# Optimization experiments

Measured on AMD Instinct MI355X. Metric: run time of the kernel, lower is better.

Reference implementation:

```python
import jax, jax.numpy as jnp
import numpy as np

N = 50000        # nodes
E = 1_600_000    # edges (avg degree 32)
D_IN = 128
HID = 256
D_OUT = 128      # must equal D_IN for the residual add


def setup_inputs() -> dict:
    key = jax.random.key(0)
    k0, k1, k2, k3 = jax.random.split(key, 4)
    x = jax.random.normal(k0, (N, D_IN), dtype=jnp.float32)
    edge_index = jax.random.randint(k1, (2, E), 0, N, dtype=jnp.int32)
    # GCNConv params (lin: Linear without bias in PyG, plus additive bias)
    W1 = jax.random.normal(k2, (D_IN, HID), dtype=jnp.float32) / np.sqrt(D_IN)
    b1 = jnp.zeros((HID,), jnp.float32)
    W2 = jax.random.normal(k3, (HID, D_OUT), dtype=jnp.float32) / np.sqrt(HID)
    b2 = jnp.zeros((D_OUT,), jnp.float32)
    return {"x": x, "edge_index": edge_index, "W1": W1, "b1": b1, "W2": W2, "b2": b2}


def _gcn_conv(x, src, dst, norm, W, b, n):
    # PyG GCNConv: transform, gather source features, scale by sym-norm, scatter-add to dst.
    h = x @ W                        # [n, d_out]
    msg = h[src] * norm[:, None]     # [E+n, d_out] gathered messages
    out = jax.ops.segment_sum(msg, dst, num_segments=n)
    return out + b


def reference(x, edge_index, W1, b1, W2, b2):
    n = x.shape[0]
    # add self loops (GCNConv default add_self_loops=True)
    loops = jnp.arange(n, dtype=edge_index.dtype)
    src = jnp.concatenate([edge_index[0], loops])
    dst = jnp.concatenate([edge_index[1], loops])
    # symmetric normalization D^{-1/2} (A+I) D^{-1/2}
    deg = jax.ops.segment_sum(jnp.ones_like(dst, dtype=x.dtype), dst, num_segments=n)
    dinv = jnp.where(deg > 0, jax.lax.rsqrt(deg), 0.0)
    norm = dinv[src] * dinv[dst]
    skip = x  # nn.Identity skip connection
    h = jax.nn.relu(_gcn_conv(x, src, dst, norm, W1, b1, n))
    out = _gcn_conv(h, src, dst, norm, W2, b2, n)
    # classification_layer treated as identity; original .double() cast kept in fp32
    return out + skip
```

## Files before the change

### kernel.cpp

```cpp
#include <hip/hip_runtime.h>

#define D_IN 128
#define HID 256
#define BKT_SHIFT 6
#define BKT_SIZE 64
#define BKT_CAP 3072
#define NBKT_MAX 1024
#define CHUNK 4096
#define PAD_SLACK 512
#define LSTR 264
#define ASTR 136

typedef __attribute__((ext_vector_type(8))) short short8;
typedef __attribute__((ext_vector_type(4))) float floatx4;
typedef __attribute__((ext_vector_type(4))) int intx4;

static __device__ __forceinline__ unsigned short f2b(float f) {
  unsigned u = __float_as_uint(f);
  unsigned r = (u + 0x7fffu + ((u >> 16) & 1u)) >> 16;
  return (unsigned short)r;
}

static __device__ __forceinline__ void unpack8(uint4 v, float* f) {
  f[0] = __uint_as_float(v.x << 16); f[1] = __uint_as_float(v.x & 0xffff0000u);
  f[2] = __uint_as_float(v.y << 16); f[3] = __uint_as_float(v.y & 0xffff0000u);
  f[4] = __uint_as_float(v.z << 16); f[5] = __uint_as_float(v.z & 0xffff0000u);
  f[6] = __uint_as_float(v.w << 16); f[7] = __uint_as_float(v.w & 0xffff0000u);
}

static __device__ __forceinline__ void acc_fma(float* acc, uint4 v, float w) {
  float g[8];
  unpack8(v, g);
#pragma unroll
  for (int d = 0; d < 8; ++d) acc[d] = fmaf(g[d], w, acc[d]);
}

static __device__ __forceinline__ void gather_row(float* acc, const uint4* __restrict__ Hq,
                                                  const float* __restrict__ dinv,
                                                  const int* __restrict__ csr,
                                                  int2 se, float dv, int lane) {
  intx4 c0 = *(const intx4*)(csr + se.x);
  intx4 c1 = *(const intx4*)(csr + se.x + 4);
  for (int j = se.x; j < se.y; ) {
    const int jn = j + 8;
    const int jp = (jn < se.y) ? jn : se.x;
    intx4 n0 = *(const intx4*)(csr + jp);
    intx4 n1 = *(const intx4*)(csr + jp + 4);
    float w0 = dinv[c0.x] * dv, w1 = dinv[c0.y] * dv;
    float w2 = dinv[c0.z] * dv, w3 = dinv[c0.w] * dv;
    float w4 = dinv[c1.x] * dv, w5 = dinv[c1.y] * dv;
    float w6 = dinv[c1.z] * dv, w7 = dinv[c1.w] * dv;
    uint4 v0 = Hq[(size_t)c0.x * 16 + lane];
    uint4 v1 = Hq[(size_t)c0.y * 16 + lane];
    uint4 v2 = Hq[(size_t)c0.z * 16 + lane];
    uint4 v3 = Hq[(size_t)c0.w * 16 + lane];
    uint4 v4 = Hq[(size_t)c1.x * 16 + lane];
    uint4 v5 = Hq[(size_t)c1.y * 16 + lane];
    uint4 v6 = Hq[(size_t)c1.z * 16 + lane];
    uint4 v7 = Hq[(size_t)c1.w * 16 + lane];
    acc_fma(acc, v0, w0);
    acc_fma(acc, v1, w1);
    acc_fma(acc, v2, w2);
    acc_fma(acc, v3, w3);
    acc_fma(acc, v4, w4);
    acc_fma(acc, v5, w5);
    acc_fma(acc, v6, w6);
    acc_fma(acc, v7, w7);
    c0 = n0; c1 = n1; j = jn;
  }
}


__global__ __launch_bounds__(256) void fused_front_kernel(
    const int* __restrict__ src, const int* __restrict__ dst,
    int* __restrict__ bkt_cursor, int* __restrict__ ebuf, int E, int nbkt, int nchunk,
    const float4* __restrict__ x4, unsigned short* __restrict__ xb, int n4,
    const float* __restrict__ W1, unsigned short* __restrict__ Wt1,
    const float* __restrict__ W2, unsigned short* __restrict__ Wt2,
    float* __restrict__ dinv, unsigned short* __restrict__ tb, int N) {
  const int bid = blockIdx.x;
  const int tid = threadIdx.x;
  if (bid < nchunk) {
    __shared__ int hist[NBKT_MAX];
    __shared__ int bbase[NBKT_MAX];
    for (int b = tid; b < nbkt; b += 256) hist[b] = 0;
    __syncthreads();
    const int base = bid * CHUNK;
    const int end = min(base + CHUNK, E);
    for (int e = base + tid; e < end; e += 256)
      atomicAdd(&hist[dst[e] >> BKT_SHIFT], 1);
    __syncthreads();
    for (int b = tid; b < nbkt; b += 256) {
      int c = hist[b];
      bbase[b] = c > 0 ? atomicAdd(&bkt_cursor[b], c) : 0;
      hist[b] = 0;
    }
    __syncthreads();
    for (int e = base + tid; e < end; e += 256) {
      int d = dst[e];
      int b = d >> BKT_SHIFT;
      int off = atomicAdd(&hist[b], 1);
      int rel = bbase[b] + off;
      if (rel < BKT_CAP)
        ebuf[b * BKT_CAP + rel] = (src[e] << BKT_SHIFT) | (d & (BKT_SIZE - 1));
    }
    return;
  }
  const int nxblk = (n4 + 255) / 256;
  if (bid < nchunk + nxblk) {
    int i = (bid - nchunk) * 256 + tid;
    if (i >= n4) return;
    float4 v = x4[i];
    ushort4 o;
    o.x = f2b(v.x); o.y = f2b(v.y); o.z = f2b(v.z); o.w = f2b(v.w);
    *(ushort4*)(xb + (size_t)i * 4) = o;
  } else if (bid < nchunk + nxblk + 128) {
    int e = (bid - nchunk - nxblk) * 256 + tid;
    int k = e >> 8, n = e & 255;
    Wt1[(size_t)n * D_IN + k] = f2b(W1[e]);
  } else if (bid < nchunk + nxblk + 256) {
    int e = (bid - nchunk - nxblk - 128) * 256 + tid;
    int k = e >> 7, n = e & 127;
    Wt2[(size_t)n * HID + k] = f2b(W2[e]);
  } else {
    if (tid == 0) dinv[N] = 0.f;
    if (tid < 64)       ((unsigned*)(xb + (size_t)N * D_IN))[tid]      = 0u;
    else if (tid < 128) ((unsigned*)(tb + (size_t)N * D_IN))[tid - 64] = 0u;
  }
}


__global__ __launch_bounds__(256) void bucket_build_kernel(const int* __restrict__ ebuf,
                                                           const int* __restrict__ bkt_cursor,
                                                           float* __restrict__ dinv,
                                                           int2* __restrict__ rowse,
                                                           int* __restrict__ csr,
                                                           int N, int nbkt) {
  __shared__ int hist[BKT_SIZE];
  __shared__ int srs[BKT_SIZE];
  const int b = blockIdx.x;
  const int tid = threadIdx.x;
  const int node0 = b << BKT_SHIFT;
  const int nloc = min(BKT_SIZE, N - node0);
  const int ebeg = b * BKT_CAP;
  const int eend = ebeg + min(bkt_cursor[b], BKT_CAP);

  if (tid < BKT_SIZE) hist[tid] = 0;
  __syncthreads();
  for (int e = ebeg + tid; e < eend; e += 256)
    atomicAdd(&hist[ebuf[e] & (BKT_SIZE - 1)], 1);
  __syncthreads();

  if (tid < BKT_SIZE) {
    const int h = hist[tid];
    const int p = (h + 7) & ~7;
    int incl = p;
#pragma unroll
    for (int off = 1; off < 64; off <<= 1) {
      int t = __shfl_up(incl, off);
      if (tid >= off) incl += t;
    }
    const int ex = incl - p;
    if (tid < nloc) {
      int st = b * (BKT_CAP + PAD_SLACK) + ex;
      dinv[node0 + tid] = rsqrtf((float)(h + 1));
      rowse[node0 + tid] = make_int2(st, st + p);
      srs[tid] = st;
    }
  }
  __syncthreads();
  if (tid < BKT_SIZE) hist[tid] = 0;
  __syncthreads();

  for (int e = ebeg + tid; e < eend; e += 256) {
    int u = ebuf[e];
    int l = u & (BKT_SIZE - 1);
    int pos = atomicAdd(&hist[l], 1);
    csr[srs[l] + pos] = u >> BKT_SHIFT;
  }
  __syncthreads();
  for (int l = tid; l < nloc; l += 256) {
    int deg = hist[l];
    int pp = (deg + 7) & ~7;
    int s0 = srs[l];
    for (int q = s0 + deg; q < s0 + pp; ++q) csr[q] = N;
  }
}


__global__ __launch_bounds__(512, 4) void agg1_gemm_kernel(
    const uint4* __restrict__ Hq, const int2* __restrict__ rowse,
    const int* __restrict__ csr, const float* __restrict__ dinv,
    const unsigned short* __restrict__ Wt1, const float* __restrict__ b1,
    const unsigned short* __restrict__ Wt2, unsigned short* __restrict__ T, int M) {
  __shared__ unsigned short as_[32][ASTR];
  __shared__ unsigned short hs[32][LSTR];
  const int tid = threadIdx.x;
  const int node0 = blockIdx.x * 32;

  {
    const int glane = tid & 15;
    const int lrow = tid >> 4;
    const int node = node0 + lrow;
    float acc[8] = {0.f, 0.f, 0.f, 0.f, 0.f, 0.f, 0.f, 0.f};
    if (node < M) {
      const float dv = dinv[node];
      uint4 sv = Hq[(size_t)node * 16 + glane];
      float f[8];
      unpack8(sv, f);
      const float ws = dv * dv;
#pragma unroll
      for (int d = 0; d < 8; ++d) acc[d] = f[d] * ws;
      gather_row(acc, Hq, dinv, csr, rowse[node], dv, glane);
    }
    uint4 o;
    o.x = (unsigned)f2b(acc[0]) | ((unsigned)f2b(acc[1]) << 16);
    o.y = (unsigned)f2b(acc[2]) | ((unsigned)f2b(acc[3]) << 16);
    o.z = (unsigned)f2b(acc[4]) | ((unsigned)f2b(acc[5]) << 16);
    o.w = (unsigned)f2b(acc[6]) | ((unsigned)f2b(acc[7]) << 16);
    *(uint4*)&as_[lrow][glane * 8] = o;
  }
  __syncthreads();

  const int wave = tid >> 6;
  const int lane = tid & 63;
  const int quad = lane >> 4;
  const int l16 = lane & 15;

  const short8* bp1 = (const short8*)(Wt1 + (size_t)(wave * 32 + l16) * D_IN + quad * 8);
  floatx4 acc1[2][2];
#pragma unroll
  for (int g = 0; g < 2; ++g)
#pragma unroll
    for (int t = 0; t < 2; ++t) acc1[g][t] = floatx4{0.f, 0.f, 0.f, 0.f};

#pragma unroll
  for (int kt = 0; kt < 4; ++kt) {
    short8 a0 = *(const short8*)&as_[0 * 16 + l16][kt * 32 + quad * 8];
    short8 a1 = *(const short8*)&as_[1 * 16 + l16][kt * 32 + quad * 8];
#pragma unroll
    for (int t = 0; t < 2; ++t) {
      short8 b = bp1[kt * 4 + t * 256];
      acc1[0][t] = __builtin_amdgcn_mfma_f32_16x16x32_bf16(a0, b, acc1[0][t], 0, 0, 0);
      acc1[1][t] = __builtin_amdgcn_mfma_f32_16x16x32_bf16(a1, b, acc1[1][t], 0, 0, 0);
    }
  }
#pragma unroll
  for (int t = 0; t < 2; ++t) {
    const float bv = b1[wave * 32 + t * 16 + l16];
#pragma unroll
    for (int g = 0; g < 2; ++g)
#pragma unroll
      for (int r = 0; r < 4; ++r) {
        float v = acc1[g][t][r] + bv;
        v = v > 0.f ? v : 0.f;
        hs[g * 16 + quad * 4 + r][wave * 32 + t * 16 + l16] = f2b(v);
      }
  }
  __syncthreads();

  const short8* bp2 = (const short8*)(Wt2 + (size_t)(wave * 16 + l16) * HID + quad * 8);
  floatx4 acc2[2];
#pragma unroll
  for (int g = 0; g < 2; ++g) acc2[g] = floatx4{0.f, 0.f, 0.f, 0.f};

#pragma unroll
  for (int kt = 0; kt < 8; ++kt) {
    short8 a0 = *(const short8*)&hs[0 * 16 + l16][kt * 32 + quad * 8];
    short8 a1 = *(const short8*)&hs[1 * 16 + l16][kt * 32 + quad * 8];
    short8 b = bp2[kt * 4];
    acc2[0] = __builtin_amdgcn_mfma_f32_16x16x32_bf16(a0, b, acc2[0], 0, 0, 0);
    acc2[1] = __builtin_amdgcn_mfma_f32_16x16x32_bf16(a1, b, acc2[1], 0, 0, 0);
  }
  __syncthreads();

#pragma unroll
  for (int g = 0; g < 2; ++g)
#pragma unroll
    for (int r = 0; r < 4; ++r)
      hs[g * 16 + quad * 4 + r][wave * 16 + l16] = f2b(acc2[g][r]);
  __syncthreads();

  {
    const int r = tid >> 4;
    const int c = (tid & 15) * 8;
    const int row = node0 + r;
    uint4 v = *(const uint4*)&hs[r][c];
    if (row < M) *(uint4*)&T[(size_t)row * D_IN + c] = v;
  }
}


__global__ __launch_bounds__(256) void agg2_kernel(const uint4* __restrict__ Hq,
                                                   const int2* __restrict__ rowse,
                                                   const int* __restrict__ csr,
                                                   const float* __restrict__ dinv,
                                                   const float* __restrict__ skip,
                                                   const float* __restrict__ bias,
                                                   float* __restrict__ OUT, int n) {
  const int lane = threadIdx.x & 15;
  const int node = blockIdx.x * 16 + (threadIdx.x >> 4);
  if (node >= n) return;

  const float dv = dinv[node];
  float acc[8];
  {
    uint4 sv = Hq[(size_t)node * 16 + lane];
    float f[8];
    unpack8(sv, f);
    const float ws = dv * dv;
#pragma unroll
    for (int d = 0; d < 8; ++d) acc[d] = f[d] * ws;
  }
  gather_row(acc, Hq, dinv, csr, rowse[node], dv, lane);

  const float* sp = skip + (size_t)node * 128 + lane * 8;
  const float* bp = bias + lane * 8;
  float4 s0 = *(const float4*)sp, s1 = *(const float4*)(sp + 4);
  float4 b0 = *(const float4*)bp, b1 = *(const float4*)(bp + 4);
  float* op = OUT + (size_t)node * 128 + lane * 8;
  *(float4*)op = make_float4(acc[0] + s0.x + b0.x, acc[1] + s0.y + b0.y,
                             acc[2] + s0.z + b0.z, acc[3] + s0.w + b0.w);
  *(float4*)(op + 4) = make_float4(acc[4] + s1.x + b1.x, acc[5] + s1.y + b1.y,
                                   acc[6] + s1.z + b1.z, acc[7] + s1.w + b1.w);
}


extern "C" void kernel_launch(void* const* d_in, const int* in_sizes, int n_in,
                              void* d_out, int out_size, void* d_ws, size_t ws_size,
                              hipStream_t stream) {
  const float* x  = (const float*)d_in[0];
  const int*   ei = (const int*)d_in[1];
  const float* W1 = (const float*)d_in[2];
  const float* b1 = (const float*)d_in[3];
  const float* W2 = (const float*)d_in[4];
  const float* b2 = (const float*)d_in[5];
  float* out = (float*)d_out;

  const int N = in_sizes[0] / D_IN;
  const int E = in_sizes[1] / 2;
  const int* srcA = ei;
  const int* dstA = ei + E;
  const int NBKT = (N + BKT_SIZE - 1) >> BKT_SHIFT;
  const int NCHUNK = (E + CHUNK - 1) / CHUNK;
  const int n4 = N * D_IN / 4;

  char* ws = (char*)d_ws;
  size_t off = 0;
  auto alloc = [&](size_t bytes) { void* p = ws + off; off = (off + bytes + 255) & ~(size_t)255; return p; };
  int*            bkt_cursor = (int*)           alloc((size_t)NBKT * 4);
  float*          dinv       = (float*)         alloc((size_t)(N + 1) * 4);
  int2*           rowse      = (int2*)          alloc((size_t)N * 8);
  int*            ebuf       = (int*)           alloc((size_t)NBKT * BKT_CAP * 4);
  int*            csr        = (int*)           alloc((size_t)NBKT * (BKT_CAP + PAD_SLACK) * 4);
  unsigned short* xb         = (unsigned short*)alloc((size_t)(N + 1) * D_IN * 2);
  unsigned short* tb         = (unsigned short*)alloc((size_t)(N + 1) * D_IN * 2);
  unsigned short* Wt1        = (unsigned short*)alloc((size_t)D_IN * HID * 2);
  unsigned short* Wt2        = (unsigned short*)alloc((size_t)D_IN * HID * 2);

  const int nxblk = (n4 + 255) / 256;

  (void)hipMemsetAsync(bkt_cursor, 0, (size_t)NBKT * 4, stream);
  fused_front_kernel<<<NCHUNK + nxblk + 256 + 1, 256, 0, stream>>>(
      srcA, dstA, bkt_cursor, ebuf, E, NBKT, NCHUNK,
      (const float4*)x, xb, n4, W1, Wt1, W2, Wt2, dinv, tb, N);
  bucket_build_kernel<<<NBKT, 256, 0, stream>>>(ebuf, bkt_cursor, dinv, rowse, csr, N, NBKT);
  agg1_gemm_kernel<<<(N + 31) / 32, 512, 0, stream>>>((const uint4*)xb, rowse, csr, dinv,
                                                      Wt1, b1, Wt2, tb, N);
  agg2_kernel<<<(N + 15) / 16, 256, 0, stream>>>((const uint4*)tb, rowse, csr,
                                                 dinv, x, b2, out, N);
}
```

Measured before the change: 267.2 us.

## Prescale features by dinv so edge gathers become plain sums

Factors the symmetric normalization as dinv[dst]*sum(dinv[src]*h[src]). Source rows are prescaled by dinv when they are written (x during bucket build, layer-2 input in the GEMM epilogue), and the destination factor is applied once per row. This removes the per-edge dinv gathers and multiplies from both aggregation kernels. The x-to-bf16 conversion moves from the front kernel into bucket_build, where dinv is already in shared memory. The cost is slightly different rounding, since scaling now happens before bf16 quantization.

```diff
diff --git a/kernel.cpp b/kernel.cpp
--- a/kernel.cpp
+++ b/kernel.cpp
@@ -28,17 +28,16 @@
   f[6] = __uint_as_float(v.w << 16); f[7] = __uint_as_float(v.w & 0xffff0000u);
 }
 
-static __device__ __forceinline__ void acc_fma(float* acc, uint4 v, float w) {
+static __device__ __forceinline__ void acc_add(float* acc, uint4 v) {
   float g[8];
   unpack8(v, g);
 #pragma unroll
-  for (int d = 0; d < 8; ++d) acc[d] = fmaf(g[d], w, acc[d]);
+  for (int d = 0; d < 8; ++d) acc[d] += g[d];
 }
 
 static __device__ __forceinline__ void gather_row(float* acc, const uint4* __restrict__ Hq,
-                                                  const float* __restrict__ dinv,
                                                   const int* __restrict__ csr,
-                                                  int2 se, float dv, int lane) {
+                                                  int2 se, int lane) {
   intx4 c0 = *(const intx4*)(csr + se.x);
   intx4 c1 = *(const intx4*)(csr + se.x + 4);
   for (int j = se.x; j < se.y; ) {
@@ -46,10 +45,6 @@
     const int jp = (jn < se.y) ? jn : se.x;
     intx4 n0 = *(const intx4*)(csr + jp);
     intx4 n1 = *(const intx4*)(csr + jp + 4);
-    float w0 = dinv[c0.x] * dv, w1 = dinv[c0.y] * dv;
-    float w2 = dinv[c0.z] * dv, w3 = dinv[c0.w] * dv;
-    float w4 = dinv[c1.x] * dv, w5 = dinv[c1.y] * dv;
-    float w6 = dinv[c1.z] * dv, w7 = dinv[c1.w] * dv;
     uint4 v0 = Hq[(size_t)c0.x * 16 + lane];
     uint4 v1 = Hq[(size_t)c0.y * 16 + lane];
     uint4 v2 = Hq[(size_t)c0.z * 16 + lane];
@@ -58,14 +53,14 @@
     uint4 v5 = Hq[(size_t)c1.y * 16 + lane];
     uint4 v6 = Hq[(size_t)c1.z * 16 + lane];
     uint4 v7 = Hq[(size_t)c1.w * 16 + lane];
-    acc_fma(acc, v0, w0);
-    acc_fma(acc, v1, w1);
-    acc_fma(acc, v2, w2);
-    acc_fma(acc, v3, w3);
-    acc_fma(acc, v4, w4);
-    acc_fma(acc, v5, w5);
-    acc_fma(acc, v6, w6);
-    acc_fma(acc, v7, w7);
+    acc_add(acc, v0);
+    acc_add(acc, v1);
+    acc_add(acc, v2);
+    acc_add(acc, v3);
+    acc_add(acc, v4);
+    acc_add(acc, v5);
+    acc_add(acc, v6);
+    acc_add(acc, v7);
     c0 = n0; c1 = n1; j = jn;
   }
 }
@@ -74,10 +69,10 @@
 __global__ __launch_bounds__(256) void fused_front_kernel(
     const int* __restrict__ src, const int* __restrict__ dst,
     int* __restrict__ bkt_cursor, int* __restrict__ ebuf, int E, int nbkt, int nchunk,
-    const float4* __restrict__ x4, unsigned short* __restrict__ xb, int n4,
     const float* __restrict__ W1, unsigned short* __restrict__ Wt1,
     const float* __restrict__ W2, unsigned short* __restrict__ Wt2,
-    float* __restrict__ dinv, unsigned short* __restrict__ tb, int N) {
+    float* __restrict__ dinv, unsigned short* __restrict__ xb,
+    unsigned short* __restrict__ tb, int N) {
   const int bid = blockIdx.x;
   const int tid = threadIdx.x;
   if (bid < nchunk) {
@@ -106,20 +101,12 @@
     }
     return;
   }
-  const int nxblk = (n4 + 255) / 256;
-  if (bid < nchunk + nxblk) {
-    int i = (bid - nchunk) * 256 + tid;
-    if (i >= n4) return;
-    float4 v = x4[i];
-    ushort4 o;
-    o.x = f2b(v.x); o.y = f2b(v.y); o.z = f2b(v.z); o.w = f2b(v.w);
-    *(ushort4*)(xb + (size_t)i * 4) = o;
-  } else if (bid < nchunk + nxblk + 128) {
-    int e = (bid - nchunk - nxblk) * 256 + tid;
+  if (bid < nchunk + 128) {
+    int e = (bid - nchunk) * 256 + tid;
     int k = e >> 8, n = e & 255;
     Wt1[(size_t)n * D_IN + k] = f2b(W1[e]);
-  } else if (bid < nchunk + nxblk + 256) {
-    int e = (bid - nchunk - nxblk - 128) * 256 + tid;
+  } else if (bid < nchunk + 256) {
+    int e = (bid - nchunk - 128) * 256 + tid;
     int k = e >> 7, n = e & 127;
     Wt2[(size_t)n * HID + k] = f2b(W2[e]);
   } else {
@@ -132,12 +119,15 @@
 
 __global__ __launch_bounds__(256) void bucket_build_kernel(const int* __restrict__ ebuf,
                                                            const int* __restrict__ bkt_cursor,
+                                                           const float4* __restrict__ x4,
+                                                           unsigned short* __restrict__ xb,
                                                            float* __restrict__ dinv,
                                                            int2* __restrict__ rowse,
                                                            int* __restrict__ csr,
                                                            int N, int nbkt) {
   __shared__ int hist[BKT_SIZE];
   __shared__ int srs[BKT_SIZE];
+  __shared__ float sdinv[BKT_SIZE];
   const int b = blockIdx.x;
   const int tid = threadIdx.x;
   const int node0 = b << BKT_SHIFT;
@@ -161,9 +151,11 @@
       if (tid >= off) incl += t;
     }
     const int ex = incl - p;
+    float dv = rsqrtf((float)(h + 1));
+    sdinv[tid] = dv;
     if (tid < nloc) {
       int st = b * (BKT_CAP + PAD_SLACK) + ex;
-      dinv[node0 + tid] = rsqrtf((float)(h + 1));
+      dinv[node0 + tid] = dv;
       rowse[node0 + tid] = make_int2(st, st + p);
       srs[tid] = st;
     }
@@ -184,6 +176,16 @@
     int pp = (deg + 7) & ~7;
     int s0 = srs[l];
     for (int q = s0 + deg; q < s0 + pp; ++q) csr[q] = N;
+  }
+
+  for (int i = tid; i < nloc * 32; i += 256) {
+    const int l = i >> 5;
+    const float dv = sdinv[l];
+    float4 v = x4[(size_t)(node0 + l) * 32 + (i & 31)];
+    ushort4 o;
+    o.x = f2b(v.x * dv); o.y = f2b(v.y * dv);
+    o.z = f2b(v.z * dv); o.w = f2b(v.w * dv);
+    *(ushort4*)(xb + (size_t)(node0 + l) * D_IN + (i & 31) * 4) = o;
   }
 }
 
@@ -203,21 +205,18 @@
     const int lrow = tid >> 4;
     const int node = node0 + lrow;
     float acc[8] = {0.f, 0.f, 0.f, 0.f, 0.f, 0.f, 0.f, 0.f};
+    float dv = 0.f;
     if (node < M) {
-      const float dv = dinv[node];
+      dv = dinv[node];
       uint4 sv = Hq[(size_t)node * 16 + glane];
-      float f[8];
-      unpack8(sv, f);
-      const float ws = dv * dv;
-#pragma unroll
-      for (int d = 0; d < 8; ++d) acc[d] = f[d] * ws;
-      gather_row(acc, Hq, dinv, csr, rowse[node], dv, glane);
+      unpack8(sv, acc);
+      gather_row(acc, Hq, csr, rowse[node], glane);
     }
     uint4 o;
-    o.x = (unsigned)f2b(acc[0]) | ((unsigned)f2b(acc[1]) << 16);
-    o.y = (unsigned)f2b(acc[2]) | ((unsigned)f2b(acc[3]) << 16);
-    o.z = (unsigned)f2b(acc[4]) | ((unsigned)f2b(acc[5]) << 16);
-    o.w = (unsigned)f2b(acc[6]) | ((unsigned)f2b(acc[7]) << 16);
+    o.x = (unsigned)f2b(acc[0] * dv) | ((unsigned)f2b(acc[1] * dv) << 16);
+    o.y = (unsigned)f2b(acc[2] * dv) | ((unsigned)f2b(acc[3] * dv) << 16);
+    o.z = (unsigned)f2b(acc[4] * dv) | ((unsigned)f2b(acc[5] * dv) << 16);
+    o.w = (unsigned)f2b(acc[6] * dv) | ((unsigned)f2b(acc[7] * dv) << 16);
     *(uint4*)&as_[lrow][glane * 8] = o;
   }
   __syncthreads();
@@ -277,8 +276,11 @@
 #pragma unroll
   for (int g = 0; g < 2; ++g)
 #pragma unroll
-    for (int r = 0; r < 4; ++r)
-      hs[g * 16 + quad * 4 + r][wave * 16 + l16] = f2b(acc2[g][r]);
+    for (int r = 0; r < 4; ++r) {
+      int rr = node0 + g * 16 + quad * 4 + r;
+      float dvr = dinv[rr < M ? rr : M];
+      hs[g * 16 + quad * 4 + r][wave * 16 + l16] = f2b(acc2[g][r] * dvr);
+    }
   __syncthreads();
 
   {
@@ -306,23 +308,19 @@
   float acc[8];
   {
     uint4 sv = Hq[(size_t)node * 16 + lane];
-    float f[8];
-    unpack8(sv, f);
-    const float ws = dv * dv;
-#pragma unroll
-    for (int d = 0; d < 8; ++d) acc[d] = f[d] * ws;
-  }
-  gather_row(acc, Hq, dinv, csr, rowse[node], dv, lane);
+    unpack8(sv, acc);
+  }
+  gather_row(acc, Hq, csr, rowse[node], lane);
 
   const float* sp = skip + (size_t)node * 128 + lane * 8;
   const float* bp = bias + lane * 8;
   float4 s0 = *(const float4*)sp, s1 = *(const float4*)(sp + 4);
   float4 b0 = *(const float4*)bp, b1 = *(const float4*)(bp + 4);
   float* op = OUT + (size_t)node * 128 + lane * 8;
-  *(float4*)op = make_float4(acc[0] + s0.x + b0.x, acc[1] + s0.y + b0.y,
-                             acc[2] + s0.z + b0.z, acc[3] + s0.w + b0.w);
-  *(float4*)(op + 4) = make_float4(acc[4] + s1.x + b1.x, acc[5] + s1.y + b1.y,
-                                   acc[6] + s1.z + b1.z, acc[7] + s1.w + b1.w);
+  *(float4*)op = make_float4(fmaf(acc[0], dv, s0.x + b0.x), fmaf(acc[1], dv, s0.y + b0.y),
+                             fmaf(acc[2], dv, s0.z + b0.z), fmaf(acc[3], dv, s0.w + b0.w));
+  *(float4*)(op + 4) = make_float4(fmaf(acc[4], dv, s1.x + b1.x), fmaf(acc[5], dv, s1.y + b1.y),
+                                   fmaf(acc[6], dv, s1.z + b1.z), fmaf(acc[7], dv, s1.w + b1.w));
 }
 
 
@@ -343,7 +341,6 @@
   const int* dstA = ei + E;
   const int NBKT = (N + BKT_SIZE - 1) >> BKT_SHIFT;
   const int NCHUNK = (E + CHUNK - 1) / CHUNK;
-  const int n4 = N * D_IN / 4;
 
   char* ws = (char*)d_ws;
   size_t off = 0;
@@ -358,13 +355,12 @@
   unsigned short* Wt1        = (unsigned short*)alloc((size_t)D_IN * HID * 2);
   unsigned short* Wt2        = (unsigned short*)alloc((size_t)D_IN * HID * 2);
 
-  const int nxblk = (n4 + 255) / 256;
-
   (void)hipMemsetAsync(bkt_cursor, 0, (size_t)NBKT * 4, stream);
-  fused_front_kernel<<<NCHUNK + nxblk + 256 + 1, 256, 0, stream>>>(
+  fused_front_kernel<<<NCHUNK + 256 + 1, 256, 0, stream>>>(
       srcA, dstA, bkt_cursor, ebuf, E, NBKT, NCHUNK,
-      (const float4*)x, xb, n4, W1, Wt1, W2, Wt2, dinv, tb, N);
-  bucket_build_kernel<<<NBKT, 256, 0, stream>>>(ebuf, bkt_cursor, dinv, rowse, csr, N, NBKT);
+      W1, Wt1, W2, Wt2, dinv, xb, tb, N);
+  bucket_build_kernel<<<NBKT, 256, 0, stream>>>(ebuf, bkt_cursor, (const float4*)x,
+                                                xb, dinv, rowse, csr, N, NBKT);
   agg1_gemm_kernel<<<(N + 31) / 32, 512, 0, stream>>>((const uint4*)xb, rowse, csr, dinv,
                                                       Wt1, b1, Wt2, tb, N);
   agg2_kernel<<<(N + 15) / 16, 256, 0, stream>>>((const uint4*)tb, rowse, csr,
```

Result: faster. 261.5 us (median of 2 runs) (-2.1%).
